# Performance work log

Hardware: AMD Instinct MI355X
Metric: run time of the kernel (lower is better)

The kernel has to match this reference:

```python
import jax, jax.numpy as jnp
import numpy as np

N = 100000      # nodes
IN = 64         # in_channels
HID = 64        # hidden_channels
H2 = HID // 2   # per-sign channels
E = 1600000     # edges per sign


def _mean_aggr(x_src, edge_index, num_nodes):
    """Mean of x_src[src] scattered onto dst (PyG mean aggregation)."""
    src, dst = edge_index[0], edge_index[1]
    s = jax.ops.segment_sum(x_src[src], dst, num_segments=num_nodes)
    cnt = jax.ops.segment_sum(jnp.ones((src.shape[0],), x_src.dtype), dst,
                              num_segments=num_nodes)
    return s / jnp.maximum(cnt, 1.0)[:, None]


def setup_inputs() -> dict:
    key = jax.random.key(0)
    ks = jax.random.split(key, 12)
    x = jax.random.normal(ks[0], (N, IN), jnp.float32)
    pos_edge_index = jax.random.randint(ks[1], (2, E), 0, N)
    neg_edge_index = jax.random.randint(ks[2], (2, E), 0, N)

    def w(k, fan_in, fan_out):
        b = 1.0 / np.sqrt(fan_in)
        return jax.random.uniform(k, (fan_in, fan_out), jnp.float32, -b, b)

    return dict(
        x=x, pos_edge_index=pos_edge_index, neg_edge_index=neg_edge_index,
        # conv1 (first_aggr=True): lin_l (no bias applied via l), lin_r (bias)
        w1_pl=w(ks[3], IN, H2), w1_pr=w(ks[4], IN, H2), b1_p=jnp.zeros((H2,), jnp.float32),
        w1_nl=w(ks[5], IN, H2), w1_nr=w(ks[6], IN, H2), b1_n=jnp.zeros((H2,), jnp.float32),
        # conv2 (first_aggr=False): lin_l over cat of two aggregations (2*H2), lin_r over H2
        w2_pl=w(ks[7], 2 * H2, H2), w2_pr=w(ks[8], H2, H2), b2_p=jnp.zeros((H2,), jnp.float32),
        w2_nl=w(ks[9], 2 * H2, H2), w2_nr=w(ks[10], H2, H2), b2_n=jnp.zeros((H2,), jnp.float32),
    )


def reference(x, pos_edge_index, neg_edge_index,
              w1_pl, w1_pr, b1_p, w1_nl, w1_nr, b1_n,
              w2_pl, w2_pr, b2_p, w2_nl, w2_nr, b2_n):
    n = x.shape[0]
    # --- conv1, first_aggr=True ---
    agg_p = _mean_aggr(x, pos_edge_index, n)          # [N, IN]
    agg_n = _mean_aggr(x, neg_edge_index, n)
    out_pos = agg_p @ w1_pl + x @ w1_pr + b1_p         # [N, H2]
    out_neg = agg_n @ w1_nl + x @ w1_nr + b1_n
    z = jax.nn.relu(jnp.concatenate([out_pos, out_neg], axis=-1))  # [N, HID]

    # --- conv2, first_aggr=False ---
    h2 = z.shape[-1] // 2
    zp, zn = z[:, :h2], z[:, h2:]
    p1 = _mean_aggr(zp, pos_edge_index, n)
    p2 = _mean_aggr(zn, neg_edge_index, n)
    out_pos = jnp.concatenate([p1, p2], axis=-1) @ w2_pl + zp @ w2_pr + b2_p
    n1 = _mean_aggr(zn, pos_edge_index, n)
    n2 = _mean_aggr(zp, neg_edge_index, n)
    out_neg = jnp.concatenate([n1, n2], axis=-1) @ w2_nl + zn @ w2_nr + b2_n
    z = jax.nn.relu(jnp.concatenate([out_pos, out_neg], axis=-1))  # [N, HID]
    return z
```

## Files before the change

kernel.cpp:

```cpp
#include <hip/hip_runtime.h>
#include <hip/hip_fp16.h>

using uint = unsigned int;

static constexpr int NN  = 100000;
static constexpr int NE  = 1600000;
static constexpr int DIM = 64;
static constexpr int HH  = 32;
static constexpr int NBLK = (NN + 255) / 256;
static constexpr int HB   = 256;
static constexpr int CHUNK = NE / HB;
static constexpr int BSH  = 9;
static constexpr int BSZ  = 512;
static constexpr int NBKT = (NN + BSZ - 1) / BSZ;

__device__ __forceinline__ float2 up16(uint v) {
  __half2 h = *reinterpret_cast<__half2*>(&v);
  return __half22float2(h);
}
__device__ __forceinline__ uint pk16(float a, float b) {
  __half2 h = __floats2half2_rn(a, b);
  return *reinterpret_cast<uint*>(&h);
}


__global__ void c_hist(const int* __restrict__ pe, const int* __restrict__ ne,
                       int* __restrict__ part_hist) {
  const int set = blockIdx.y;
  const int* dstA = (set ? ne : pe) + NE;
  __shared__ int h[256];
  h[threadIdx.x] = 0;
  __syncthreads();
  int lo = blockIdx.x * CHUNK;
  int hi = lo + CHUNK;
  for (int i = lo + threadIdx.x; i < hi; i += 256)
    atomicAdd(&h[dstA[i] >> BSH], 1);
  __syncthreads();
  part_hist[(size_t)(set * HB + blockIdx.x) * 256 + threadIdx.x] = h[threadIdx.x];
}

__global__ void c_colscan(int* __restrict__ part_hist, int* __restrict__ tot) {
  const int set = blockIdx.y;
  const int k   = blockIdx.x;
  const int t   = threadIdx.x;
  int v = part_hist[(size_t)(set * HB + t) * 256 + k];
  __shared__ int sm[256];
  sm[t] = v;
  __syncthreads();
  for (int off = 1; off < 256; off <<= 1) {
    int add = (t >= off) ? sm[t - off] : 0;
    __syncthreads();
    sm[t] += add;
    __syncthreads();
  }
  part_hist[(size_t)(set * HB + t) * 256 + k] = (t == 0) ? 0 : sm[t - 1];
  if (t == 255) tot[set * 256 + k] = sm[255];
}

__global__ void c_basescan(const int* __restrict__ tot, int* __restrict__ base) {
  const int t   = threadIdx.x;
  const int seg = t >> 8;
  const int idx = t & 255;
  int v = tot[seg * 256 + idx];
  __shared__ int sm[512];
  sm[t] = v;
  __syncthreads();
  for (int off = 1; off < 256; off <<= 1) {
    int add = (idx >= off) ? sm[t - off] : 0;
    __syncthreads();
    sm[t] += add;
    __syncthreads();
  }
  base[seg * 257 + idx] = (idx == 0) ? 0 : sm[t - 1];
  if (idx == 255) base[seg * 257 + 256] = sm[t];
}

__global__ void c_scatter(const int* __restrict__ pe, const int* __restrict__ ne,
                          const int* __restrict__ part_hist, const int* __restrict__ base,
                          uint* __restrict__ partP, uint* __restrict__ partN) {
  const int set = blockIdx.y;
  const int b   = blockIdx.x;
  const int* srcA = set ? ne : pe;
  const int* dstA = srcA + NE;
  uint* part = set ? partN : partP;
  __shared__ int off[256];
  const int* ph = part_hist + (size_t)(set * HB + b) * 256;
  off[threadIdx.x] = base[set * 257 + threadIdx.x] + ph[threadIdx.x];
  __syncthreads();
  int lo = b * CHUNK;
  int hi = lo + CHUNK;
  for (int i = lo + threadIdx.x; i < hi; i += 256) {
    int src = srcA[i];
    int dst = dstA[i];
    int pos = atomicAdd(&off[dst >> BSH], 1);
    part[pos] = ((uint)src << BSH) | (uint)(dst & (BSZ - 1));
  }
}

__global__ void c_bucket(const uint* __restrict__ partP, const uint* __restrict__ partN,
                         const int* __restrict__ base,
                         int* __restrict__ row_p, int* __restrict__ row_n,
                         int* __restrict__ col_p, int* __restrict__ col_n) {
  const int bx = blockIdx.x;
  const int t  = threadIdx.x;
  const int set = (bx >= NBKT) ? 1 : 0;
  const int k   = bx - (set ? NBKT : 0);
  const uint* part = set ? partN : partP;
  int* row = set ? row_n : row_p;
  int* col = set ? col_n : col_p;
  const int lo = k * BSZ;
  const int hi = min(lo + BSZ, NN);
  const int s = base[set * 257 + k];
  const int e = base[set * 257 + k + 1];

  __shared__ int cnt[BSZ], rowl[BSZ], cnt2[BSZ];
  cnt[t] = 0; cnt2[t] = 0;
  __syncthreads();
  for (int i = s + t; i < e; i += 512)
    atomicAdd(&cnt[part[i] & (BSZ - 1)], 1);
  __syncthreads();
  rowl[t] = cnt[t];
  __syncthreads();
  for (int off = 1; off < BSZ; off <<= 1) {
    int a0 = (t >= off) ? rowl[t - off] : 0;
    __syncthreads();
    rowl[t] += a0;
    __syncthreads();
  }
  if (lo + t < hi) row[lo + t] = s + (t ? rowl[t - 1] : 0);
  if (k == NBKT - 1 && t == 0) row[NN] = NE;
  for (int i = s + t; i < e; i += 512) {
    uint p = part[i];
    int l = p & (BSZ - 1);
    int pos = s + (l ? rowl[l - 1] : 0) + atomicAdd(&cnt2[l], 1);
    col[pos] = (int)(p >> BSH);
  }
}

__global__ void k_pre1(const float* __restrict__ x,
                       const float* __restrict__ w1_pl, const float* __restrict__ w1_pr,
                       const float* __restrict__ b1_p,
                       const float* __restrict__ w1_nl, const float* __restrict__ w1_nr,
                       const float* __restrict__ b1_n,
                       uint* __restrict__ y1p, uint* __restrict__ y1n,
                       float* __restrict__ r1) {
  const int h = blockIdx.y;
  const float* wl   = h ? w1_nl : w1_pl;
  const float* wr   = h ? w1_nr : w1_pr;
  const float* bias = h ? b1_n  : b1_p;

  __shared__ float s_wl[DIM * HH];
  __shared__ float s_wr[DIM * HH];
  for (int i = threadIdx.x; i < DIM * HH; i += 256) {
    s_wl[i] = wl[i];
    s_wr[i] = wr[i];
  }
  __syncthreads();

  int node = blockIdx.x * 256 + threadIdx.x;
  if (node >= NN) return;

  float ay[HH], ar[HH];
#pragma unroll
  for (int j = 0; j < HH; ++j) { ay[j] = 0.f; ar[j] = bias[j]; }

  const float4* xrow = (const float4*)(x + (size_t)node * DIM);
#pragma unroll 4
  for (int k4 = 0; k4 < DIM / 4; ++k4) {
    float4 xv = xrow[k4];
#pragma unroll
    for (int u = 0; u < 4; ++u) {
      int k = k4 * 4 + u;
      float xk = (&xv.x)[u];
#pragma unroll
      for (int j = 0; j < HH; ++j) {
        ay[j] += xk * s_wl[k * HH + j];
        ar[j] += xk * s_wr[k * HH + j];
      }
    }
  }

  uint*  yo = (h ? y1n : y1p) + (size_t)node * 16;
  float* ro = r1 + (size_t)node * 64 + h * 32;
#pragma unroll
  for (int j = 0; j < 16; ++j) yo[j] = pk16(ay[2 * j], ay[2 * j + 1]);
#pragma unroll
  for (int j = 0; j < HH; ++j) ro[j] = ar[j];
}

__global__ void k_aggr1(const uint* __restrict__ y1p, const uint* __restrict__ y1n,
                        const int* __restrict__ rp, const int* __restrict__ cp,
                        const int* __restrict__ rn, const int* __restrict__ cn,
                        const float* r1,
                        float* z) {
  int gid  = blockIdx.x * 256 + threadIdx.x;
  int node = gid >> 6;
  if (node >= NN) return;
  int lane = threadIdx.x & 63;
  int g = lane >> 2;
  int f = lane & 3;

  int s = rp[node], e = rp[node + 1];
  float a[8];
#pragma unroll
  for (int j = 0; j < 8; ++j) a[j] = 0.f;
  for (int i = s + g; i < e; i += 16) {
    int c = cp[i];
    uint4 v = *(const uint4*)&y1p[(size_t)c * 16 + 4 * f];
    float2 p0 = up16(v.x), p1 = up16(v.y), p2 = up16(v.z), p3 = up16(v.w);
    a[0] += p0.x; a[1] += p0.y; a[2] += p1.x; a[3] += p1.y;
    a[4] += p2.x; a[5] += p2.y; a[6] += p3.x; a[7] += p3.y;
  }
#pragma unroll
  for (int w = 4; w <= 32; w <<= 1) {
#pragma unroll
    for (int j = 0; j < 8; ++j) a[j] += __shfl_xor(a[j], w);
  }
  float invp = 1.f / (float)max(e - s, 1);

  s = rn[node]; e = rn[node + 1];
  float b[8];
#pragma unroll
  for (int j = 0; j < 8; ++j) b[j] = 0.f;
  for (int i = s + g; i < e; i += 16) {
    int c = cn[i];
    uint4 v = *(const uint4*)&y1n[(size_t)c * 16 + 4 * f];
    float2 p0 = up16(v.x), p1 = up16(v.y), p2 = up16(v.z), p3 = up16(v.w);
    b[0] += p0.x; b[1] += p0.y; b[2] += p1.x; b[3] += p1.y;
    b[4] += p2.x; b[5] += p2.y; b[6] += p3.x; b[7] += p3.y;
  }
#pragma unroll
  for (int w = 4; w <= 32; w <<= 1) {
#pragma unroll
    for (int j = 0; j < 8; ++j) b[j] += __shfl_xor(b[j], w);
  }
  float invn = 1.f / (float)max(e - s, 1);

  size_t base = (size_t)node * 64;
  if (g == 0) {
    const float4 r0 = *(const float4*)(r1 + base + 8 * f);
    const float4 r1v = *(const float4*)(r1 + base + 8 * f + 4);
    float4 o0, o1;
    o0.x = fmaxf(a[0] * invp + r0.x, 0.f);
    o0.y = fmaxf(a[1] * invp + r0.y, 0.f);
    o0.z = fmaxf(a[2] * invp + r0.z, 0.f);
    o0.w = fmaxf(a[3] * invp + r0.w, 0.f);
    o1.x = fmaxf(a[4] * invp + r1v.x, 0.f);
    o1.y = fmaxf(a[5] * invp + r1v.y, 0.f);
    o1.z = fmaxf(a[6] * invp + r1v.z, 0.f);
    o1.w = fmaxf(a[7] * invp + r1v.w, 0.f);
    *(float4*)(z + base + 8 * f) = o0;
    *(float4*)(z + base + 8 * f + 4) = o1;
  } else if (g == 1) {
    const float4 r0 = *(const float4*)(r1 + base + 32 + 8 * f);
    const float4 r1v = *(const float4*)(r1 + base + 32 + 8 * f + 4);
    float4 o0, o1;
    o0.x = fmaxf(b[0] * invn + r0.x, 0.f);
    o0.y = fmaxf(b[1] * invn + r0.y, 0.f);
    o0.z = fmaxf(b[2] * invn + r0.z, 0.f);
    o0.w = fmaxf(b[3] * invn + r0.w, 0.f);
    o1.x = fmaxf(b[4] * invn + r1v.x, 0.f);
    o1.y = fmaxf(b[5] * invn + r1v.y, 0.f);
    o1.z = fmaxf(b[6] * invn + r1v.z, 0.f);
    o1.w = fmaxf(b[7] * invn + r1v.w, 0.f);
    *(float4*)(z + base + 32 + 8 * f) = o0;
    *(float4*)(z + base + 32 + 8 * f + 4) = o1;
  }
}

__global__ void k_mid(const float* __restrict__ z,
                      const float* __restrict__ w2_pl, const float* __restrict__ w2_pr,
                      const float* __restrict__ b2_p,
                      const float* __restrict__ w2_nl, const float* __restrict__ w2_nr,
                      const float* __restrict__ b2_n,
                      uint* __restrict__ u_pos, uint* __restrict__ u_neg,
                      float* __restrict__ r2) {
  const int t = blockIdx.y;
  const float* mat;
  const float* bias = nullptr;
  int srcHalf;
  switch (t) {
    case 0: mat = w2_pl;            srcHalf = 0; break;
    case 1: mat = w2_nl;            srcHalf = 1; break;
    case 2: mat = w2_pl + 32 * 32;  srcHalf = 1; break;
    case 3: mat = w2_nl + 32 * 32;  srcHalf = 0; break;
    case 4: mat = w2_pr; bias = b2_p; srcHalf = 0; break;
    default: mat = w2_nr; bias = b2_n; srcHalf = 1; break;
  }

  __shared__ float s_m[HH][HH];
  for (int i = threadIdx.x; i < HH * HH; i += 256) s_m[i >> 5][i & 31] = mat[i];
  __syncthreads();

  int node = blockIdx.x * 256 + threadIdx.x;
  if (node >= NN) return;

  float acc[HH];
#pragma unroll
  for (int j = 0; j < HH; ++j) acc[j] = bias ? bias[j] : 0.f;

  const float4* zrow = (const float4*)(z + (size_t)node * 64 + srcHalf * 32);
#pragma unroll 4
  for (int k4 = 0; k4 < HH / 4; ++k4) {
    float4 v = zrow[k4];
#pragma unroll
    for (int u = 0; u < 4; ++u) {
      int k = k4 * 4 + u;
      float vv = (&v.x)[u];
#pragma unroll
      for (int j = 0; j < HH; ++j) acc[j] += vv * s_m[k][j];
    }
  }

  if (t < 4) {
    uint* o = (t < 2 ? u_pos : u_neg) + (size_t)node * 32 + (t & 1) * 16;
#pragma unroll
    for (int j = 0; j < 16; ++j) o[j] = pk16(acc[2 * j], acc[2 * j + 1]);
  } else {
    float* o = r2 + (size_t)node * 64 + (t - 4) * 32;
#pragma unroll
    for (int j = 0; j < HH; ++j) o[j] = acc[j];
  }
}

__global__ void k_aggr2(const uint* __restrict__ u_pos, const uint* __restrict__ u_neg,
                        const int* __restrict__ rp, const int* __restrict__ cp,
                        const int* __restrict__ rn, const int* __restrict__ cn,
                        const float* __restrict__ r2,
                        float* __restrict__ out) {
  int gid  = blockIdx.x * 256 + threadIdx.x;
  int node = gid >> 6;
  if (node >= NN) return;
  int lane = threadIdx.x & 63;
  int g = lane >> 3;
  int f = lane & 7;

  int s = rp[node], e = rp[node + 1];
  float a[8];
#pragma unroll
  for (int j = 0; j < 8; ++j) a[j] = 0.f;
  for (int i = s + g; i < e; i += 8) {
    int c = cp[i];
    uint4 v = *(const uint4*)&u_pos[(size_t)c * 32 + 4 * f];
    float2 p0 = up16(v.x), p1 = up16(v.y), p2 = up16(v.z), p3 = up16(v.w);
    a[0] += p0.x; a[1] += p0.y; a[2] += p1.x; a[3] += p1.y;
    a[4] += p2.x; a[5] += p2.y; a[6] += p3.x; a[7] += p3.y;
  }
#pragma unroll
  for (int w = 8; w <= 32; w <<= 1) {
#pragma unroll
    for (int j = 0; j < 8; ++j) a[j] += __shfl_xor(a[j], w);
  }
  float invp = 1.f / (float)max(e - s, 1);

  s = rn[node]; e = rn[node + 1];
  float b[8];
#pragma unroll
  for (int j = 0; j < 8; ++j) b[j] = 0.f;
  for (int i = s + g; i < e; i += 8) {
    int c = cn[i];
    uint4 v = *(const uint4*)&u_neg[(size_t)c * 32 + 4 * f];
    float2 p0 = up16(v.x), p1 = up16(v.y), p2 = up16(v.z), p3 = up16(v.w);
    b[0] += p0.x; b[1] += p0.y; b[2] += p1.x; b[3] += p1.y;
    b[4] += p2.x; b[5] += p2.y; b[6] += p3.x; b[7] += p3.y;
  }
#pragma unroll
  for (int w = 8; w <= 32; w <<= 1) {
#pragma unroll
    for (int j = 0; j < 8; ++j) b[j] += __shfl_xor(b[j], w);
  }
  float invn = 1.f / (float)max(e - s, 1);

  if (g == 0) {
    size_t base = (size_t)node * 64 + 8 * f;
    const float4 r0 = *(const float4*)(r2 + base);
    const float4 r1v = *(const float4*)(r2 + base + 4);
    float4 o0, o1;
    o0.x = fmaxf(a[0] * invp + b[0] * invn + r0.x, 0.f);
    o0.y = fmaxf(a[1] * invp + b[1] * invn + r0.y, 0.f);
    o0.z = fmaxf(a[2] * invp + b[2] * invn + r0.z, 0.f);
    o0.w = fmaxf(a[3] * invp + b[3] * invn + r0.w, 0.f);
    o1.x = fmaxf(a[4] * invp + b[4] * invn + r1v.x, 0.f);
    o1.y = fmaxf(a[5] * invp + b[5] * invn + r1v.y, 0.f);
    o1.z = fmaxf(a[6] * invp + b[6] * invn + r1v.z, 0.f);
    o1.w = fmaxf(a[7] * invp + b[7] * invn + r1v.w, 0.f);
    *(float4*)(out + base) = o0;
    *(float4*)(out + base + 4) = o1;
  }
}


extern "C" void kernel_launch(void* const* d_in, const int* in_sizes, int n_in,
                              void* d_out, int out_size, void* d_ws, size_t ws_size,
                              hipStream_t stream) {
  const float* x     = (const float*)d_in[0];
  const int*   pe    = (const int*)d_in[1];
  const int*   ne    = (const int*)d_in[2];
  const float* w1_pl = (const float*)d_in[3];
  const float* w1_pr = (const float*)d_in[4];
  const float* b1_p  = (const float*)d_in[5];
  const float* w1_nl = (const float*)d_in[6];
  const float* w1_nr = (const float*)d_in[7];
  const float* b1_n  = (const float*)d_in[8];
  const float* w2_pl = (const float*)d_in[9];
  const float* w2_pr = (const float*)d_in[10];
  const float* b2_p  = (const float*)d_in[11];
  const float* w2_nl = (const float*)d_in[12];
  const float* w2_nr = (const float*)d_in[13];
  const float* b2_n  = (const float*)d_in[14];

  char* ws = (char*)d_ws;
  size_t off = 0;
  auto alloc = [&](size_t bytes) -> char* {
    char* p = ws + off;
    off = (off + bytes + 255) & ~(size_t)255;
    return p;
  };

  int* row_p = (int*)alloc((size_t)(NN + 1) * 4);
  int* row_n = (int*)alloc((size_t)(NN + 1) * 4);
  int* col_p = (int*)alloc((size_t)NE * 4);
  int* col_n = (int*)alloc((size_t)NE * 4);
  int* tot   = (int*)alloc((size_t)2 * 256 * 4);
  int* base  = (int*)alloc((size_t)2 * 257 * 4);

  char* regA  = alloc((size_t)NN * 64 * 4);
  uint* partP = (uint*)regA;
  uint* partN = (uint*)(regA + (size_t)NE * 4);
  int*  part_hist = (int*)(regA + (size_t)2 * NE * 4);
  uint* u_pos = (uint*)regA;
  uint* u_neg = (uint*)(regA + (size_t)NN * 32 * 4);

  char*  regB = alloc((size_t)NN * 64 * 4);
  uint*  y1p  = (uint*)regB;
  uint*  y1n  = (uint*)(regB + (size_t)NN * 16 * 4);
  float* r2   = (float*)regB;

  float* r1 = (float*)d_out;
  float* z  = (float*)d_out;

  const int nb = NBLK;
  const int ab = (NN * 64 + 255) / 256;

  dim3 pg(nb, 2);
  k_pre1<<<pg, 256, 0, stream>>>(x, w1_pl, w1_pr, b1_p, w1_nl, w1_nr, b1_n,
                                 y1p, y1n, r1);

  dim3 hg(HB, 2);
  c_hist<<<hg, 256, 0, stream>>>(pe, ne, part_hist);
  dim3 cg(256, 2);
  c_colscan<<<cg, 256, 0, stream>>>(part_hist, tot);
  c_basescan<<<1, 512, 0, stream>>>(tot, base);
  c_scatter<<<hg, 256, 0, stream>>>(pe, ne, part_hist, base, partP, partN);
  c_bucket<<<2 * NBKT, 512, 0, stream>>>(partP, partN, base,
                                         row_p, row_n, col_p, col_n);

  k_aggr1<<<ab, 256, 0, stream>>>(y1p, y1n, row_p, col_p, row_n, col_n, r1, z);

  dim3 g2(nb, 6);
  k_mid<<<g2, 256, 0, stream>>>(z, w2_pl, w2_pr, b2_p, w2_nl, w2_nr, b2_n,
                                u_pos, u_neg, r2);

  k_aggr2<<<ab, 256, 0, stream>>>(u_pos, u_neg, row_p, col_p, row_n, col_n, r2,
                                  (float*)d_out);
}
```

Baseline: 299.8 us.

## Fuse first-layer projection into CSR bucket kernel and interleave y1 features

The separate k_pre1 launch is removed. Its dense first-layer projection now runs as extra blocks of the c_bucket kernel, so the GEMV work shares a launch with the CSR bucketing and can overlap with it. y1p and y1n are interleaved into one y1u array, so each node's pos and neg projections sit on adjacent cache lines for the gathers in aggr1. part_hist moves to its own buffer because regB/regA aliasing would otherwise conflict now that pre1 runs later. The costs are that the fused kernel's projection blocks run with 512 threads and share memory sizing with bucket blocks, which may reduce occupancy.

```diff
diff --git a/kernel.cpp b/kernel.cpp
--- a/kernel.cpp
+++ b/kernel.cpp
@@ -7,7 +7,7 @@
 static constexpr int NE  = 1600000;
 static constexpr int DIM = 64;
 static constexpr int HH  = 32;
-static constexpr int NBLK = (NN + 255) / 256;
+static constexpr int NBLK = (NN + 511) / 512;
 static constexpr int HB   = 256;
 static constexpr int CHUNK = NE / HB;
 static constexpr int BSH  = 9;
@@ -100,64 +100,71 @@
 __global__ void c_bucket(const uint* __restrict__ partP, const uint* __restrict__ partN,
                          const int* __restrict__ base,
                          int* __restrict__ row_p, int* __restrict__ row_n,
-                         int* __restrict__ col_p, int* __restrict__ col_n) {
+                         int* __restrict__ col_p, int* __restrict__ col_n,
+                         const float* __restrict__ x,
+                         const float* __restrict__ w1_pl, const float* __restrict__ w1_pr,
+                         const float* __restrict__ b1_p,
+                         const float* __restrict__ w1_nl, const float* __restrict__ w1_nr,
+                         const float* __restrict__ b1_n,
+                         uint* __restrict__ y1u, float* __restrict__ r1) {
+  __shared__ uint smem[4096];
   const int bx = blockIdx.x;
   const int t  = threadIdx.x;
-  const int set = (bx >= NBKT) ? 1 : 0;
-  const int k   = bx - (set ? NBKT : 0);
-  const uint* part = set ? partN : partP;
-  int* row = set ? row_n : row_p;
-  int* col = set ? col_n : col_p;
-  const int lo = k * BSZ;
-  const int hi = min(lo + BSZ, NN);
-  const int s = base[set * 257 + k];
-  const int e = base[set * 257 + k + 1];
-
-  __shared__ int cnt[BSZ], rowl[BSZ], cnt2[BSZ];
-  cnt[t] = 0; cnt2[t] = 0;
-  __syncthreads();
-  for (int i = s + t; i < e; i += 512)
-    atomicAdd(&cnt[part[i] & (BSZ - 1)], 1);
-  __syncthreads();
-  rowl[t] = cnt[t];
-  __syncthreads();
-  for (int off = 1; off < BSZ; off <<= 1) {
-    int a0 = (t >= off) ? rowl[t - off] : 0;
-    __syncthreads();
-    rowl[t] += a0;
-    __syncthreads();
-  }
-  if (lo + t < hi) row[lo + t] = s + (t ? rowl[t - 1] : 0);
-  if (k == NBKT - 1 && t == 0) row[NN] = NE;
-  for (int i = s + t; i < e; i += 512) {
-    uint p = part[i];
-    int l = p & (BSZ - 1);
-    int pos = s + (l ? rowl[l - 1] : 0) + atomicAdd(&cnt2[l], 1);
-    col[pos] = (int)(p >> BSH);
-  }
-}
-
-__global__ void k_pre1(const float* __restrict__ x,
-                       const float* __restrict__ w1_pl, const float* __restrict__ w1_pr,
-                       const float* __restrict__ b1_p,
-                       const float* __restrict__ w1_nl, const float* __restrict__ w1_nr,
-                       const float* __restrict__ b1_n,
-                       uint* __restrict__ y1p, uint* __restrict__ y1n,
-                       float* __restrict__ r1) {
-  const int h = blockIdx.y;
+
+  if (bx < 2 * NBKT) {
+    const int set = (bx >= NBKT) ? 1 : 0;
+    const int k   = bx - (set ? NBKT : 0);
+    const uint* part = set ? partN : partP;
+    int* row = set ? row_n : row_p;
+    int* col = set ? col_n : col_p;
+    const int lo = k * BSZ;
+    const int hi = min(lo + BSZ, NN);
+    const int s = base[set * 257 + k];
+    const int e = base[set * 257 + k + 1];
+
+    int* cnt  = (int*)smem;
+    int* rowl = (int*)smem + 512;
+    int* cnt2 = (int*)smem + 1024;
+    cnt[t] = 0; cnt2[t] = 0;
+    __syncthreads();
+    for (int i = s + t; i < e; i += 512)
+      atomicAdd(&cnt[part[i] & (BSZ - 1)], 1);
+    __syncthreads();
+    rowl[t] = cnt[t];
+    __syncthreads();
+    for (int off = 1; off < BSZ; off <<= 1) {
+      int a0 = (t >= off) ? rowl[t - off] : 0;
+      __syncthreads();
+      rowl[t] += a0;
+      __syncthreads();
+    }
+    if (lo + t < hi) row[lo + t] = s + (t ? rowl[t - 1] : 0);
+    if (k == NBKT - 1 && t == 0) row[NN] = NE;
+    for (int i = s + t; i < e; i += 512) {
+      uint p = part[i];
+      int l = p & (BSZ - 1);
+      int pos = s + (l ? rowl[l - 1] : 0) + atomicAdd(&cnt2[l], 1);
+      col[pos] = (int)(p >> BSH);
+    }
+    return;
+  }
+
+  const int pb   = bx - 2 * NBKT;
+  const int h    = (pb >= NBLK) ? 1 : 0;
+  const int nblk = pb - (h ? NBLK : 0);
   const float* wl   = h ? w1_nl : w1_pl;
   const float* wr   = h ? w1_nr : w1_pr;
   const float* bias = h ? b1_n  : b1_p;
 
-  __shared__ float s_wl[DIM * HH];
-  __shared__ float s_wr[DIM * HH];
-  for (int i = threadIdx.x; i < DIM * HH; i += 256) {
+  float* s_wl = (float*)smem;
+  float* s_wr = (float*)smem + 2048;
+  for (int i = t; i < DIM * HH; i += 512) {
     s_wl[i] = wl[i];
     s_wr[i] = wr[i];
   }
   __syncthreads();
 
-  int node = blockIdx.x * 256 + threadIdx.x;
+  int node = nblk * 512 + t;
   if (node >= NN) return;
 
   float ay[HH], ar[HH];
@@ -180,15 +187,15 @@
     }
   }
 
-  uint*  yo = (h ? y1n : y1p) + (size_t)node * 16;
-  float* ro = r1 + (size_t)node * 64 + h * 32;
+  uint*  yo = y1u + (size_t)node * 32 + h * 16;
+  float* ro = r1  + (size_t)node * 64 + h * 32;
 #pragma unroll
   for (int j = 0; j < 16; ++j) yo[j] = pk16(ay[2 * j], ay[2 * j + 1]);
 #pragma unroll
   for (int j = 0; j < HH; ++j) ro[j] = ar[j];
 }
 
-__global__ void k_aggr1(const uint* __restrict__ y1p, const uint* __restrict__ y1n,
+__global__ void k_aggr1(const uint* __restrict__ y1u,
                         const int* __restrict__ rp, const int* __restrict__ cp,
                         const int* __restrict__ rn, const int* __restrict__ cn,
                         const float* r1,
@@ -206,7 +213,7 @@
   for (int j = 0; j < 8; ++j) a[j] = 0.f;
   for (int i = s + g; i < e; i += 16) {
     int c = cp[i];
-    uint4 v = *(const uint4*)&y1p[(size_t)c * 16 + 4 * f];
+    uint4 v = *(const uint4*)&y1u[(size_t)c * 32 + 4 * f];
     float2 p0 = up16(v.x), p1 = up16(v.y), p2 = up16(v.z), p3 = up16(v.w);
     a[0] += p0.x; a[1] += p0.y; a[2] += p1.x; a[3] += p1.y;
     a[4] += p2.x; a[5] += p2.y; a[6] += p3.x; a[7] += p3.y;
@@ -224,7 +231,7 @@
   for (int j = 0; j < 8; ++j) b[j] = 0.f;
   for (int i = s + g; i < e; i += 16) {
     int c = cn[i];
-    uint4 v = *(const uint4*)&y1n[(size_t)c * 16 + 4 * f];
+    uint4 v = *(const uint4*)&y1u[(size_t)c * 32 + 16 + 4 * f];
     float2 p0 = up16(v.x), p1 = up16(v.y), p2 = up16(v.z), p3 = up16(v.w);
     b[0] += p0.x; b[1] += p0.y; b[2] += p1.x; b[3] += p1.y;
     b[4] += p2.x; b[5] += p2.y; b[6] += p3.x; b[7] += p3.y;
@@ -421,30 +428,25 @@
   int* row_n = (int*)alloc((size_t)(NN + 1) * 4);
   int* col_p = (int*)alloc((size_t)NE * 4);
   int* col_n = (int*)alloc((size_t)NE * 4);
+  int* part_hist = (int*)alloc((size_t)2 * HB * 256 * 4);
   int* tot   = (int*)alloc((size_t)2 * 256 * 4);
   int* base  = (int*)alloc((size_t)2 * 257 * 4);
 
   char* regA  = alloc((size_t)NN * 64 * 4);
   uint* partP = (uint*)regA;
   uint* partN = (uint*)(regA + (size_t)NE * 4);
-  int*  part_hist = (int*)(regA + (size_t)2 * NE * 4);
   uint* u_pos = (uint*)regA;
   uint* u_neg = (uint*)(regA + (size_t)NN * 32 * 4);
 
   char*  regB = alloc((size_t)NN * 64 * 4);
-  uint*  y1p  = (uint*)regB;
-  uint*  y1n  = (uint*)(regB + (size_t)NN * 16 * 4);
+  uint*  y1u  = (uint*)regB;
   float* r2   = (float*)regB;
 
   float* r1 = (float*)d_out;
   float* z  = (float*)d_out;
 
-  const int nb = NBLK;
+  const int nb = (NN + 255) / 256;
   const int ab = (NN * 64 + 255) / 256;
-
-  dim3 pg(nb, 2);
-  k_pre1<<<pg, 256, 0, stream>>>(x, w1_pl, w1_pr, b1_p, w1_nl, w1_nr, b1_n,
-                                 y1p, y1n, r1);
 
   dim3 hg(HB, 2);
   c_hist<<<hg, 256, 0, stream>>>(pe, ne, part_hist);
@@ -452,10 +454,11 @@
   c_colscan<<<cg, 256, 0, stream>>>(part_hist, tot);
   c_basescan<<<1, 512, 0, stream>>>(tot, base);
   c_scatter<<<hg, 256, 0, stream>>>(pe, ne, part_hist, base, partP, partN);
-  c_bucket<<<2 * NBKT, 512, 0, stream>>>(partP, partN, base,
-                                         row_p, row_n, col_p, col_n);
-
-  k_aggr1<<<ab, 256, 0, stream>>>(y1p, y1n, row_p, col_p, row_n, col_n, r1, z);
+  c_bucket<<<2 * NBKT + 2 * NBLK, 512, 0, stream>>>(
+      partP, partN, base, row_p, row_n, col_p, col_n,
+      x, w1_pl, w1_pr, b1_p, w1_nl, w1_nr, b1_n, y1u, r1);
+
+  k_aggr1<<<ab, 256, 0, stream>>>(y1u, row_p, col_p, row_n, col_n, r1, z);
 
   dim3 g2(nb, 6);
   k_mid<<<g2, 256, 0, stream>>>(z, w2_pl, w2_pr, b2_p, w2_nl, w2_nr, b2_n,
```

After: 297.8 us, median of 2. Within noise of the previous version (-0.6%).
